# Optimization experiments

Measured on AMD Instinct MI355X. Metric: run time of the kernel, lower is better.

## Reference

```python
import jax, jax.numpy as jnp
import numpy as np

INIT_RANGE = 0.02

def setup_inputs() -> dict:
    key = jax.random.key(0)
    ks = jax.random.split(key, 5)
    B, S, D, H, Dh = 4, 2048, 768, 12, 64
    residual = jax.random.normal(ks[0], (B, S, D), dtype=jnp.float32)
    W_Q = jax.random.normal(ks[1], (H, D, Dh), dtype=jnp.float32) * INIT_RANGE
    W_K = jax.random.normal(ks[2], (H, D, Dh), dtype=jnp.float32) * INIT_RANGE
    W_V = jax.random.normal(ks[3], (H, D, Dh), dtype=jnp.float32) * INIT_RANGE
    W_O = jax.random.normal(ks[4], (H, Dh, D), dtype=jnp.float32) * INIT_RANGE
    b_Q = jnp.zeros((H, Dh), dtype=jnp.float32)
    b_K = jnp.zeros((H, Dh), dtype=jnp.float32)
    b_V = jnp.zeros((H, Dh), dtype=jnp.float32)
    b_O = jnp.zeros((D,), dtype=jnp.float32)
    return {"residual": residual, "W_Q": W_Q, "W_K": W_K, "W_V": W_V,
            "W_O": W_O, "b_Q": b_Q, "b_K": b_K, "b_V": b_V, "b_O": b_O}

def reference(residual, W_Q, W_K, W_V, W_O, b_Q, b_K, b_V, b_O):
    # residual: [b, s, d]; W_{Q,K,V}: [h, d, dh]; W_O: [h, dh, d]
    d_head = W_Q.shape[-1]
    q = jnp.einsum('bsd,hde->bshe', residual, W_Q) + b_Q  # [b, s, h, dh]
    k = jnp.einsum('bsd,hde->bshe', residual, W_K) + b_K
    v = jnp.einsum('bsd,hde->bshe', residual, W_V) + b_V
    scores = jnp.einsum('bqhe,bkhe->bhqk', q, k) / jnp.sqrt(jnp.float32(d_head))
    S = residual.shape[1]
    causal = jnp.tril(jnp.ones((S, S), dtype=bool))  # True where attending allowed
    scores = jnp.where(causal, scores, -jnp.inf)
    pattern = jax.nn.softmax(scores, axis=-1)  # [b, h, q, k]
    z = jnp.einsum('bkhe,bhqk->bqhe', v, pattern)  # [b, q, h, dh]
    attn_out = jnp.einsum('bqhe,hed->bqd', z, W_O) + b_O
    return attn_out
```

## Files before the change

kernel.cpp:

```cpp
#include <hip/hip_runtime.h>

typedef short short8 __attribute__((ext_vector_type(8)));
typedef float floatx4 __attribute__((ext_vector_type(4)));
typedef unsigned short ushort_t;


__device__ inline ushort_t f2bf(float f) {
  union { float f; unsigned u; } x; x.f = f;
  unsigned u = x.u;
  unsigned r = u + 0x7fffu + ((u >> 16) & 1u);
  return (ushort_t)(r >> 16);
}

__device__ inline unsigned cvtpk(float a, float b) {
  unsigned r;
  asm("v_cvt_pk_bf16_f32 %0, %1, %2" : "=v"(r) : "v"(a), "v"(b));
  return r;
}

__device__ inline float fexp2(float x) {
#if __has_builtin(__builtin_amdgcn_exp2f)
  return __builtin_amdgcn_exp2f(x);
#else
  return exp2f(x);
#endif
}

__device__ inline void async16(const void* g, void* l) {
  __builtin_amdgcn_global_load_lds((const __attribute__((address_space(1))) void*)g,
                                   (__attribute__((address_space(3))) void*)l,
                                   16, 0, 0);
}


__global__ __launch_bounds__(256) void conv_prep(
    const float* __restrict__ x, ushort_t* __restrict__ rx,
    const float* __restrict__ wq, const float* __restrict__ wk, const float* __restrict__ wv,
    const float* __restrict__ wo,
    const float* __restrict__ bq, const float* __restrict__ bk, const float* __restrict__ bv,
    ushort_t* __restrict__ wqkvT, ushort_t* __restrict__ woT, float* __restrict__ bqkv)
{
  __shared__ ushort_t t[64 * 72];
  const int tid = threadIdx.x;
  const int bid0 = blockIdx.x;
  if (bid0 < 6144) {
    int i = bid0 * 256 + tid;
    float4 f = ((const float4*)x)[i];
    ushort4 o;
    o.x = f2bf(f.x); o.y = f2bf(f.y); o.z = f2bf(f.z); o.w = f2bf(f.w);
    ((ushort4*)rx)[i] = o;
    return;
  }
  const int bid = bid0 - 6144;
  if (bid < 432) {
    int m = bid / 144, rem = bid % 144;
    int h = rem / 12, dt = rem % 12;
    int d0 = dt * 64;
    const float* w = (m == 0) ? wq : ((m == 1) ? wk : wv);
    const float* src = w + ((size_t)h * 768 + d0) * 64;
#pragma unroll
    for (int i = 0; i < 4; ++i) {
      int task = i * 256 + tid;
      int row = task >> 4, c4 = task & 15;
      float4 f = *(const float4*)(src + row * 64 + c4 * 4);
      ushort4 o4;
      o4.x = f2bf(f.x); o4.y = f2bf(f.y); o4.z = f2bf(f.z); o4.w = f2bf(f.w);
      *(ushort4*)&t[row * 72 + c4 * 4] = o4;
    }
    __syncthreads();
    ushort_t* dst = wqkvT + ((size_t)m * 768 + h * 64) * 768 + d0;
#pragma unroll
    for (int i = 0; i < 2; ++i) {
      int task = i * 256 + tid;
      int e = task >> 3, sc = task & 7;
      short8 d8;
#pragma unroll
      for (int j = 0; j < 8; ++j) d8[j] = (short)t[(sc * 8 + j) * 72 + e];
      *(short8*)(dst + (size_t)e * 768 + sc * 8) = d8;
    }
  } else if (bid < 576) {
    int b2 = bid - 432;
    int het = b2 / 12, dt = b2 % 12;
    int he0 = het * 64, d0 = dt * 64;
    const float* src = wo + (size_t)he0 * 768 + d0;
#pragma unroll
    for (int i = 0; i < 4; ++i) {
      int task = i * 256 + tid;
      int row = task >> 4, c4 = task & 15;
      float4 f = *(const float4*)(src + (size_t)row * 768 + c4 * 4);
      ushort4 o4;
      o4.x = f2bf(f.x); o4.y = f2bf(f.y); o4.z = f2bf(f.z); o4.w = f2bf(f.w);
      *(ushort4*)&t[row * 72 + c4 * 4] = o4;
    }
    __syncthreads();
    ushort_t* dst = woT + (size_t)d0 * 768 + he0;
#pragma unroll
    for (int i = 0; i < 2; ++i) {
      int task = i * 256 + tid;
      int dd = task >> 3, sc = task & 7;
      short8 d8;
#pragma unroll
      for (int j = 0; j < 8; ++j) d8[j] = (short)t[(sc * 8 + j) * 72 + dd];
      *(short8*)(dst + (size_t)dd * 768 + sc * 8) = d8;
    }
  } else {
    for (int idx = tid; idx < 2304; idx += 256) {
      int m = idx / 768, rem = idx - m * 768;
      const float* bp = (m == 0) ? bq : ((m == 1) ? bk : bv);
      bqkv[idx] = bp[rem];
    }
  }
}


__global__ __launch_bounds__(256) void gemm_qkv(
    const ushort_t* __restrict__ A, const ushort_t* __restrict__ Bt,
    const float* __restrict__ bias,
    ushort_t* __restrict__ q, ushort_t* __restrict__ k, ushort_t* __restrict__ vt)
{
  __shared__ ushort_t sh[17408];
  const int tid = threadIdx.x;
  const int wave = tid >> 6, lane = tid & 63;
  const int ln15 = lane & 15, quad = lane >> 4;
  const int id = blockIdx.x;
  const int xk = id & 7, j = id >> 3;
  const int bx = (xk >> 1) * 16 + (j & 15);
  const int by = (xk & 1) * 9 + (j >> 4);
  const int row0 = bx * 128, col0 = by * 128;
  const int wm = (wave >> 1) * 64, wn = (wave & 1) * 64;
  const int c0 = wave * 2;

  const ushort_t* gA0 = A + (size_t)(row0 + c0 * 16 + (lane >> 2)) * 768 + (lane & 3) * 8;
  const ushort_t* gB0 = Bt + (size_t)(col0 + c0 * 16 + (lane >> 2)) * 768 + (lane & 3) * 8;

  floatx4 acc[4][4];
#pragma unroll
  for (int mi = 0; mi < 4; ++mi)
#pragma unroll
    for (int ni = 0; ni < 4; ++ni)
      acc[mi][ni] = (floatx4){0.f, 0.f, 0.f, 0.f};

  async16(gA0, &sh[c0 * 512]);
  async16(gA0 + 16 * 768, &sh[c0 * 512 + 512]);
  async16(gB0, &sh[8192 + c0 * 512]);
  async16(gB0 + 16 * 768, &sh[8192 + c0 * 512 + 512]);
  __syncthreads();

  for (int kt = 0; kt < 24; ++kt) {
    const int buf = kt & 1;
    if (kt + 1 < 24) {
      ushort_t* dA = &sh[(buf ^ 1) * 4096];
      ushort_t* dB = &sh[8192 + (buf ^ 1) * 4096];
      async16(gA0 + (kt + 1) * 32, dA + c0 * 512);
      async16(gA0 + (kt + 1) * 32 + 16 * 768, dA + c0 * 512 + 512);
      async16(gB0 + (kt + 1) * 32, dB + c0 * 512);
      async16(gB0 + (kt + 1) * 32 + 16 * 768, dB + c0 * 512 + 512);
    }
    const ushort_t* sA = &sh[buf * 4096];
    const ushort_t* sB = &sh[8192 + buf * 4096];
    short8 af[4], bfv[4];
#pragma unroll
    for (int mi = 0; mi < 4; ++mi)
      af[mi] = *(const short8*)&sA[(wm + mi * 16 + ln15) * 32 + quad * 8];
#pragma unroll
    for (int ni = 0; ni < 4; ++ni)
      bfv[ni] = *(const short8*)&sB[(wn + ni * 16 + ln15) * 32 + quad * 8];
#pragma unroll
    for (int mi = 0; mi < 4; ++mi)
#pragma unroll
      for (int ni = 0; ni < 4; ++ni)
        acc[mi][ni] = __builtin_amdgcn_mfma_f32_16x16x32_bf16(af[mi], bfv[ni], acc[mi][ni], 0, 0, 0);
    __syncthreads();
  }

  if (col0 < 1536) {
    const float qscale = 0.125f * 1.44269504f;
#pragma unroll
    for (int mi = 0; mi < 4; ++mi) {
#pragma unroll
      for (int ni = 0; ni < 4; ++ni) {
        int gr = row0 + wm + mi * 16 + quad * 4;
        int gc = col0 + wn + ni * 16 + ln15;
        float bia = bias[gc];
        int m = gc / 768;
        int rem = gc - m * 768;
        int h = rem >> 6, e = rem & 63;
        ushort_t* dp = (m == 0) ? q : k;
#pragma unroll
        for (int r = 0; r < 4; ++r) {
          float val = acc[mi][ni][r] + bia;
          int rr = gr + r;
          int bb = rr >> 11, ss = rr & 2047;
          size_t dst = ((size_t)((bb * 12 + h) * 2048 + ss) << 6) + e;
          dp[dst] = f2bf((m == 0) ? val * qscale : val);
        }
      }
    }
  } else {
#pragma unroll
    for (int mi = 0; mi < 4; ++mi) {
#pragma unroll
      for (int ni = 0; ni < 4; ++ni) {
        int col = wn + ni * 16 + ln15;
        int rowb = wm + mi * 16 + quad * 4;
        float bia = bias[col0 + col];
        ushort4 w4;
        w4.x = f2bf(acc[mi][ni][0] + bia);
        w4.y = f2bf(acc[mi][ni][1] + bia);
        w4.z = f2bf(acc[mi][ni][2] + bia);
        w4.w = f2bf(acc[mi][ni][3] + bia);
        *(ushort4*)&sh[col * 136 + rowb] = w4;
      }
    }
    __syncthreads();
    const int relc0 = col0 - 1536;
    const int bb = row0 >> 11, s0 = row0 & 2047;
#pragma unroll
    for (int i = 0; i < 8; ++i) {
      int g = i * 256 + tid;
      int col = g >> 4, chunk = g & 15;
      short8 d = *(const short8*)&sh[col * 136 + chunk * 8];
      int hh = (relc0 + col) >> 6;
      int ee = col & 63;
      *(short8*)(vt + (((size_t)(bb * 12 + hh) * 64 + ee) << 11) + s0 + chunk * 8) = d;
    }
  }
}


__global__ __launch_bounds__(256) void gemm_out(
    const ushort_t* __restrict__ A, const ushort_t* __restrict__ Bt,
    const float* __restrict__ bias, float* __restrict__ outf)
{
  __shared__ ushort_t lA[2][64 * 32];
  __shared__ ushort_t lB[2][128 * 32];
  const int tid = threadIdx.x;
  const int wave = tid >> 6, lane = tid & 63;
  const int ln15 = lane & 15, quad = lane >> 4;
  const int id = blockIdx.x;
  const int xk = id & 7, j = id >> 3;
  const int bx = xk * 16 + (j & 15);
  const int by = j >> 4;
  const int row0 = bx * 64, col0 = by * 128;
  const int wm = (wave >> 1) * 32, wn = (wave & 1) * 64;
  const int cb = wave * 2;

  const ushort_t* gA0 = A + (size_t)(row0 + wave * 16 + (lane >> 2)) * 768 + (lane & 3) * 8;
  const ushort_t* gB0 = Bt + (size_t)(col0 + cb * 16 + (lane >> 2)) * 768 + (lane & 3) * 8;

  floatx4 acc[2][4];
#pragma unroll
  for (int mi = 0; mi < 2; ++mi)
#pragma unroll
    for (int ni = 0; ni < 4; ++ni)
      acc[mi][ni] = (floatx4){0.f, 0.f, 0.f, 0.f};

  async16(gA0, &lA[0][wave * 512]);
  async16(gB0, &lB[0][cb * 512]);
  async16(gB0 + 16 * 768, &lB[0][cb * 512 + 512]);
  __syncthreads();

  for (int kt = 0; kt < 24; ++kt) {
    const int buf = kt & 1;
    if (kt + 1 < 24) {
      async16(gA0 + (kt + 1) * 32, &lA[buf ^ 1][wave * 512]);
      async16(gB0 + (kt + 1) * 32, &lB[buf ^ 1][cb * 512]);
      async16(gB0 + (kt + 1) * 32 + 16 * 768, &lB[buf ^ 1][cb * 512 + 512]);
    }
    short8 af[2], bfv[4];
#pragma unroll
    for (int mi = 0; mi < 2; ++mi)
      af[mi] = *(const short8*)&lA[buf][(wm + mi * 16 + ln15) * 32 + quad * 8];
#pragma unroll
    for (int ni = 0; ni < 4; ++ni)
      bfv[ni] = *(const short8*)&lB[buf][(wn + ni * 16 + ln15) * 32 + quad * 8];
#pragma unroll
    for (int mi = 0; mi < 2; ++mi)
#pragma unroll
      for (int ni = 0; ni < 4; ++ni)
        acc[mi][ni] = __builtin_amdgcn_mfma_f32_16x16x32_bf16(af[mi], bfv[ni], acc[mi][ni], 0, 0, 0);
    __syncthreads();
  }

#pragma unroll
  for (int mi = 0; mi < 2; ++mi) {
#pragma unroll
    for (int ni = 0; ni < 4; ++ni) {
      int gr = row0 + wm + mi * 16 + quad * 4;
      int gc = col0 + wn + ni * 16 + ln15;
      float bia = bias[gc];
#pragma unroll
      for (int r = 0; r < 4; ++r)
        outf[(size_t)(gr + r) * 768 + gc] = acc[mi][ni][r] + bia;
    }
  }
}


__device__ inline short8 frag_ld(const ushort_t* t, int row, int ch) {
  return *(const short8*)&t[row * 64 + (((ch ^ row) & 7) * 8)];
}

__global__ __launch_bounds__(256) void attn3(
    const ushort_t* __restrict__ Q, const ushort_t* __restrict__ K,
    const ushort_t* __restrict__ VT, ushort_t* __restrict__ Z)
{
  __shared__ ushort_t lK[2][64 * 64];
  __shared__ ushort_t lV[2][64 * 64];
  const int tid = threadIdx.x;
  const int wave = tid >> 6, lane = tid & 63;
  const int ln15 = lane & 15, quad = lane >> 4;
  const int bi = blockIdx.x;
  const int bh = bi % 48;
  const int t = 15 - (bi / 48);
  const int h = bh % 12, b = bh / 12;
  const size_t base = (size_t)bh * 2048 * 64;
  const ushort_t* Qp = Q + base + (size_t)t * 128 * 64;
  const ushort_t* Kp = K + base;
  const ushort_t* Vp = VT + base;
  const int nk = 2 * t + 2;

  const int srow = tid >> 3, slch = tid & 7;
  const int sc_ = slch ^ (srow & 7);
  const int krow = (srow & 3) | ((srow & 0x0C) << 1) | ((srow & 0x10) >> 2);

#pragma unroll
  for (int i = 0; i < 4; ++i) {
    int task = i * 256 + tid;
    int row = task >> 3;
    int c = slch ^ (row & 7);
    ushort_t* qdst = (row < 64) ? &lK[1][row * 64 + slch * 8]
                                : &lV[1][(row - 64) * 64 + slch * 8];
    async16(Qp + row * 64 + c * 8, qdst);
  }
  async16(Kp + (size_t)krow * 64 + sc_ * 8, &lK[0][tid * 8]);
  async16(Kp + (size_t)(krow + 32) * 64 + sc_ * 8, &lK[0][(256 + tid) * 8]);
  async16(Vp + (size_t)srow * 2048 + sc_ * 8, &lV[0][tid * 8]);
  async16(Vp + (size_t)(srow + 32) * 2048 + sc_ * 8, &lV[0][(256 + tid) * 8]);

  const ushort_t* kPre0 = Kp + (size_t)(64 + krow) * 64 + sc_ * 8;
  const ushort_t* kPre1 = kPre0 + 32 * 64;
  const ushort_t* vPre0 = Vp + (size_t)srow * 2048 + 64 + sc_ * 8;
  const ushort_t* vPre1 = vPre0 + 32 * 2048;

  __syncthreads();
  const ushort_t* qbase = (wave < 2) ? &lK[1][0] : &lV[1][0];
  const int qrl = (wave & 1) * 32;
  short8 qf[2][2];
#pragma unroll
  for (int c = 0; c < 2; ++c) {
    qf[c][0] = frag_ld(qbase, qrl + c * 16 + ln15, quad);
    qf[c][1] = frag_ld(qbase, qrl + c * 16 + ln15, quad + 4);
  }
  __syncthreads();

  float l_i[2] = {0.f, 0.f};
  floatx4 o[2][4];
#pragma unroll
  for (int c = 0; c < 2; ++c)
#pragma unroll
    for (int et = 0; et < 4; ++et) o[c][et] = (floatx4){0.f, 0.f, 0.f, 0.f};

  const int qg0 = t * 128 + wave * 32 + ln15;

  for (int kt = 0; kt < nk; ++kt) {
    const int buf = kt & 1;
    if (kt + 1 < nk) {
      ushort_t* dK = lK[buf ^ 1];
      ushort_t* dV = lV[buf ^ 1];
      async16(kPre0, dK + tid * 8);
      async16(kPre1, dK + (256 + tid) * 8);
      async16(vPre0, dV + tid * 8);
      async16(vPre1, dV + (256 + tid) * 8);
      kPre0 += 4096; kPre1 += 4096; vPre0 += 64; vPre1 += 64;
    }

    floatx4 st[2][4];
#pragma unroll
    for (int ni = 0; ni < 4; ++ni) {
      short8 kf0 = frag_ld(lK[buf], ni * 16 + ln15, quad);
      short8 kf1 = frag_ld(lK[buf], ni * 16 + ln15, quad + 4);
#pragma unroll
      for (int c = 0; c < 2; ++c) {
        floatx4 z4 = (floatx4){0.f, 0.f, 0.f, 0.f};
        z4 = __builtin_amdgcn_mfma_f32_16x16x32_bf16(kf0, qf[c][0], z4, 0, 0, 0);
        st[c][ni] = __builtin_amdgcn_mfma_f32_16x16x32_bf16(kf1, qf[c][1], z4, 0, 0, 0);
      }
    }

    const bool masked = (kt >= 2 * t);
    short8 pf[2][2];
#pragma unroll
    for (int c = 0; c < 2; ++c) {
      const int qg = qg0 + c * 16;
      float p[16];
      float rs = 0.f;
#pragma unroll
      for (int ni = 0; ni < 4; ++ni) {
#pragma unroll
        for (int r = 0; r < 4; ++r) {
          float x = st[c][ni][r];
          if (masked) {
            int kg = kt * 64 + (ni >> 1) * 32 + quad * 8 + (ni & 1) * 4 + r;
            x = (kg <= qg) ? x : -1e30f;
          }
          p[ni * 4 + r] = fexp2(x);
        }
        rs += (p[ni * 4 + 0] + p[ni * 4 + 1]) + (p[ni * 4 + 2] + p[ni * 4 + 3]);
      }
      rs += __shfl_xor(rs, 16);
      rs += __shfl_xor(rs, 32);
      l_i[c] += rs;
      union { unsigned u[4]; short8 s8; } w0, w1;
#pragma unroll
      for (int i2 = 0; i2 < 4; ++i2) {
        w0.u[i2] = cvtpk(p[i2 * 2], p[i2 * 2 + 1]);
        w1.u[i2] = cvtpk(p[8 + i2 * 2], p[8 + i2 * 2 + 1]);
      }
      pf[c][0] = w0.s8;
      pf[c][1] = w1.s8;
    }

#pragma unroll
    for (int et = 0; et < 4; ++et) {
      short8 vf0 = frag_ld(lV[buf], et * 16 + ln15, quad);
      short8 vf1 = frag_ld(lV[buf], et * 16 + ln15, quad + 4);
#pragma unroll
      for (int c = 0; c < 2; ++c) {
        o[c][et] = __builtin_amdgcn_mfma_f32_16x16x32_bf16(vf0, pf[c][0], o[c][et], 0, 0, 0);
        o[c][et] = __builtin_amdgcn_mfma_f32_16x16x32_bf16(vf1, pf[c][1], o[c][et], 0, 0, 0);
      }
    }
    __syncthreads();
  }

#pragma unroll
  for (int c = 0; c < 2; ++c) {
    float inv = 1.f / l_i[c];
    size_t zrow = (size_t)(b * 2048 + t * 128 + wave * 32 + c * 16 + ln15);
#pragma unroll
    for (int et = 0; et < 4; ++et) {
      ushort4 w;
      w.x = f2bf(o[c][et][0] * inv);
      w.y = f2bf(o[c][et][1] * inv);
      w.z = f2bf(o[c][et][2] * inv);
      w.w = f2bf(o[c][et][3] * inv);
      *(ushort4*)&Z[zrow * 768 + h * 64 + et * 16 + quad * 4] = w;
    }
  }
}


extern "C" void kernel_launch(void* const* d_in, const int* in_sizes, int n_in,
                              void* d_out, int out_size, void* d_ws, size_t ws_size,
                              hipStream_t stream)
{
  const float* residual = (const float*)d_in[0];
  const float* W_Q = (const float*)d_in[1];
  const float* W_K = (const float*)d_in[2];
  const float* W_V = (const float*)d_in[3];
  const float* W_O = (const float*)d_in[4];
  const float* b_Q = (const float*)d_in[5];
  const float* b_K = (const float*)d_in[6];
  const float* b_V = (const float*)d_in[7];
  const float* b_O = (const float*)d_in[8];
  float* out = (float*)d_out;

  char* w = (char*)d_ws;
  ushort_t* rx    = (ushort_t*)(w + 0);
  ushort_t* wqkvT = (ushort_t*)(w + 12582912);
  ushort_t* woT   = (ushort_t*)(w + 16121856);
  float*    bqkv  = (float*)   (w + 17301504);
  ushort_t* q     = (ushort_t*)(w + 17310720);
  ushort_t* k     = (ushort_t*)(w + 29893632);
  ushort_t* vt    = (ushort_t*)(w + 55059456);
  ushort_t* z     = rx;

  conv_prep<<<6721, 256, 0, stream>>>(residual, rx, W_Q, W_K, W_V, W_O,
                                      b_Q, b_K, b_V, wqkvT, woT, bqkv);
  gemm_qkv<<<1152, 256, 0, stream>>>(rx, wqkvT, bqkv, q, k, vt);
  attn3<<<768, 256, 0, stream>>>(q, k, vt, z);
  gemm_out<<<768, 256, 0, stream>>>(z, woT, b_O, out);
}
```

Baseline: 210.0 us.

## Double GEMM K-tile to 64 and XOR-swizzle LDS layouts in projection kernels

Both the QKV and output projection GEMMs now stage 64-wide K tiles instead of 32, halving the main-loop iteration and barrier count. The shared-memory tiles use an XOR swizzle of 16-byte chunks, applied to the global load addresses and to the fragment reads, to avoid LDS bank conflicts. The V-transpose staging buffer drops its padding in favour of a swizzled layout. In exchange, LDS usage per block grows, which may reduce occupancy.

```diff
diff --git a/kernel.cpp b/kernel.cpp
--- a/kernel.cpp
+++ b/kernel.cpp
@@ -118,7 +118,7 @@
     const float* __restrict__ bias,
     ushort_t* __restrict__ q, ushort_t* __restrict__ k, ushort_t* __restrict__ vt)
 {
-  __shared__ ushort_t sh[17408];
+  __shared__ __align__(16) ushort_t sh[32768];
   const int tid = threadIdx.x;
   const int wave = tid >> 6, lane = tid & 63;
   const int ln15 = lane & 15, quad = lane >> 4;
@@ -128,10 +128,17 @@
   const int by = (xk & 1) * 9 + (j >> 4);
   const int row0 = bx * 128, col0 = by * 128;
   const int wm = (wave >> 1) * 64, wn = (wave & 1) * 64;
-  const int c0 = wave * 2;
-
-  const ushort_t* gA0 = A + (size_t)(row0 + c0 * 16 + (lane >> 2)) * 768 + (lane & 3) * 8;
-  const ushort_t* gB0 = Bt + (size_t)(col0 + c0 * 16 + (lane >> 2)) * 768 + (lane & 3) * 8;
+
+  const int sr = tid >> 3;
+  const int sc = (tid & 7) ^ (sr & 7);
+  const ushort_t* gA0 = A + (size_t)(row0 + sr) * 768 + sc * 8;
+  const ushort_t* gB0 = Bt + (size_t)(col0 + sr) * 768 + sc * 8;
+
+  const int l7 = ln15 & 7;
+  const int baA = (wm + ln15) * 64;
+  const int baB = (wn + ln15) * 64;
+  const int sl0 = (quad ^ l7) * 8;
+  const int sl1 = ((quad + 4) ^ l7) * 8;
 
   floatx4 acc[4][4];
 #pragma unroll
@@ -140,36 +147,46 @@
     for (int ni = 0; ni < 4; ++ni)
       acc[mi][ni] = (floatx4){0.f, 0.f, 0.f, 0.f};
 
-  async16(gA0, &sh[c0 * 512]);
-  async16(gA0 + 16 * 768, &sh[c0 * 512 + 512]);
-  async16(gB0, &sh[8192 + c0 * 512]);
-  async16(gB0 + 16 * 768, &sh[8192 + c0 * 512 + 512]);
+#pragma unroll
+  for (int i = 0; i < 4; ++i) {
+    async16(gA0 + i * 32 * 768, &sh[(i * 256 + tid) * 8]);
+    async16(gB0 + i * 32 * 768, &sh[16384 + (i * 256 + tid) * 8]);
+  }
   __syncthreads();
 
-  for (int kt = 0; kt < 24; ++kt) {
+  for (int kt = 0; kt < 12; ++kt) {
     const int buf = kt & 1;
-    if (kt + 1 < 24) {
-      ushort_t* dA = &sh[(buf ^ 1) * 4096];
-      ushort_t* dB = &sh[8192 + (buf ^ 1) * 4096];
-      async16(gA0 + (kt + 1) * 32, dA + c0 * 512);
-      async16(gA0 + (kt + 1) * 32 + 16 * 768, dA + c0 * 512 + 512);
-      async16(gB0 + (kt + 1) * 32, dB + c0 * 512);
-      async16(gB0 + (kt + 1) * 32 + 16 * 768, dB + c0 * 512 + 512);
-    }
-    const ushort_t* sA = &sh[buf * 4096];
-    const ushort_t* sB = &sh[8192 + buf * 4096];
-    short8 af[4], bfv[4];
+    if (kt + 1 < 12) {
+      ushort_t* dA = &sh[(buf ^ 1) * 8192];
+      ushort_t* dB = &sh[16384 + (buf ^ 1) * 8192];
+      const ushort_t* ga = gA0 + (kt + 1) * 64;
+      const ushort_t* gb = gB0 + (kt + 1) * 64;
+#pragma unroll
+      for (int i = 0; i < 4; ++i) {
+        async16(ga + i * 32 * 768, dA + (i * 256 + tid) * 8);
+        async16(gb + i * 32 * 768, dB + (i * 256 + tid) * 8);
+      }
+    }
+    const ushort_t* sA = &sh[buf * 8192];
+    const ushort_t* sB = &sh[16384 + buf * 8192];
+    short8 af[4][2], bfv[4][2];
+#pragma unroll
+    for (int mi = 0; mi < 4; ++mi) {
+      af[mi][0] = *(const short8*)&sA[baA + mi * 1024 + sl0];
+      af[mi][1] = *(const short8*)&sA[baA + mi * 1024 + sl1];
+    }
+#pragma unroll
+    for (int ni = 0; ni < 4; ++ni) {
+      bfv[ni][0] = *(const short8*)&sB[baB + ni * 1024 + sl0];
+      bfv[ni][1] = *(const short8*)&sB[baB + ni * 1024 + sl1];
+    }
 #pragma unroll
     for (int mi = 0; mi < 4; ++mi)
-      af[mi] = *(const short8*)&sA[(wm + mi * 16 + ln15) * 32 + quad * 8];
-#pragma unroll
-    for (int ni = 0; ni < 4; ++ni)
-      bfv[ni] = *(const short8*)&sB[(wn + ni * 16 + ln15) * 32 + quad * 8];
-#pragma unroll
-    for (int mi = 0; mi < 4; ++mi)
-#pragma unroll
-      for (int ni = 0; ni < 4; ++ni)
-        acc[mi][ni] = __builtin_amdgcn_mfma_f32_16x16x32_bf16(af[mi], bfv[ni], acc[mi][ni], 0, 0, 0);
+#pragma unroll
+      for (int ni = 0; ni < 4; ++ni) {
+        acc[mi][ni] = __builtin_amdgcn_mfma_f32_16x16x32_bf16(af[mi][0], bfv[ni][0], acc[mi][ni], 0, 0, 0);
+        acc[mi][ni] = __builtin_amdgcn_mfma_f32_16x16x32_bf16(af[mi][1], bfv[ni][1], acc[mi][ni], 0, 0, 0);
+      }
     __syncthreads();
   }
 
@@ -203,13 +220,15 @@
       for (int ni = 0; ni < 4; ++ni) {
         int col = wn + ni * 16 + ln15;
         int rowb = wm + mi * 16 + quad * 4;
+        int rowc = rowb >> 2;
+        int msw = (col & 7) << 2;
         float bia = bias[col0 + col];
         ushort4 w4;
         w4.x = f2bf(acc[mi][ni][0] + bia);
         w4.y = f2bf(acc[mi][ni][1] + bia);
         w4.z = f2bf(acc[mi][ni][2] + bia);
         w4.w = f2bf(acc[mi][ni][3] + bia);
-        *(ushort4*)&sh[col * 136 + rowb] = w4;
+        *(ushort4*)&sh[col * 128 + ((rowc ^ msw) << 2)] = w4;
       }
     }
     __syncthreads();
@@ -219,7 +238,8 @@
     for (int i = 0; i < 8; ++i) {
       int g = i * 256 + tid;
       int col = g >> 4, chunk = g & 15;
-      short8 d = *(const short8*)&sh[col * 136 + chunk * 8];
+      int msw = (col & 7) << 2;
+      short8 d = *(const short8*)&sh[col * 128 + (((chunk * 2) ^ msw) << 2)];
       int hh = (relc0 + col) >> 6;
       int ee = col & 63;
       *(short8*)(vt + (((size_t)(bb * 12 + hh) * 64 + ee) << 11) + s0 + chunk * 8) = d;
@@ -232,8 +252,7 @@
     const ushort_t* __restrict__ A, const ushort_t* __restrict__ Bt,
     const float* __restrict__ bias, float* __restrict__ outf)
 {
-  __shared__ ushort_t lA[2][64 * 32];
-  __shared__ ushort_t lB[2][128 * 32];
+  __shared__ __align__(16) ushort_t sh[24576];
   const int tid = threadIdx.x;
   const int wave = tid >> 6, lane = tid & 63;
   const int ln15 = lane & 15, quad = lane >> 4;
@@ -243,10 +262,17 @@
   const int by = j >> 4;
   const int row0 = bx * 64, col0 = by * 128;
   const int wm = (wave >> 1) * 32, wn = (wave & 1) * 64;
-  const int cb = wave * 2;
-
-  const ushort_t* gA0 = A + (size_t)(row0 + wave * 16 + (lane >> 2)) * 768 + (lane & 3) * 8;
-  const ushort_t* gB0 = Bt + (size_t)(col0 + cb * 16 + (lane >> 2)) * 768 + (lane & 3) * 8;
+
+  const int sr = tid >> 3;
+  const int sc = (tid & 7) ^ (sr & 7);
+  const ushort_t* gA0 = A + (size_t)(row0 + sr) * 768 + sc * 8;
+  const ushort_t* gB0 = Bt + (size_t)(col0 + sr) * 768 + sc * 8;
+
+  const int l7 = ln15 & 7;
+  const int baA = (wm + ln15) * 64;
+  const int baB = (wn + ln15) * 64;
+  const int sl0 = (quad ^ l7) * 8;
+  const int sl1 = ((quad + 4) ^ l7) * 8;
 
   floatx4 acc[2][4];
 #pragma unroll
@@ -255,30 +281,48 @@
     for (int ni = 0; ni < 4; ++ni)
       acc[mi][ni] = (floatx4){0.f, 0.f, 0.f, 0.f};
 
-  async16(gA0, &lA[0][wave * 512]);
-  async16(gB0, &lB[0][cb * 512]);
-  async16(gB0 + 16 * 768, &lB[0][cb * 512 + 512]);
+#pragma unroll
+  for (int i = 0; i < 2; ++i)
+    async16(gA0 + i * 32 * 768, &sh[(i * 256 + tid) * 8]);
+#pragma unroll
+  for (int i = 0; i < 4; ++i)
+    async16(gB0 + i * 32 * 768, &sh[8192 + (i * 256 + tid) * 8]);
   __syncthreads();
 
-  for (int kt = 0; kt < 24; ++kt) {
+  for (int kt = 0; kt < 12; ++kt) {
     const int buf = kt & 1;
-    if (kt + 1 < 24) {
-      async16(gA0 + (kt + 1) * 32, &lA[buf ^ 1][wave * 512]);
-      async16(gB0 + (kt + 1) * 32, &lB[buf ^ 1][cb * 512]);
-      async16(gB0 + (kt + 1) * 32 + 16 * 768, &lB[buf ^ 1][cb * 512 + 512]);
-    }
-    short8 af[2], bfv[4];
+    if (kt + 1 < 12) {
+      ushort_t* dA = &sh[(buf ^ 1) * 4096];
+      ushort_t* dB = &sh[8192 + (buf ^ 1) * 8192];
+      const ushort_t* ga = gA0 + (kt + 1) * 64;
+      const ushort_t* gb = gB0 + (kt + 1) * 64;
+#pragma unroll
+      for (int i = 0; i < 2; ++i)
+        async16(ga + i * 32 * 768, dA + (i * 256 + tid) * 8);
+#pragma unroll
+      for (int i = 0; i < 4; ++i)
+        async16(gb + i * 32 * 768, dB + (i * 256 + tid) * 8);
+    }
+    const ushort_t* sA = &sh[buf * 4096];
+    const ushort_t* sB = &sh[8192 + buf * 8192];
+    short8 af[2][2], bfv[4][2];
+#pragma unroll
+    for (int mi = 0; mi < 2; ++mi) {
+      af[mi][0] = *(const short8*)&sA[baA + mi * 1024 + sl0];
+      af[mi][1] = *(const short8*)&sA[baA + mi * 1024 + sl1];
+    }
+#pragma unroll
+    for (int ni = 0; ni < 4; ++ni) {
+      bfv[ni][0] = *(const short8*)&sB[baB + ni * 1024 + sl0];
+      bfv[ni][1] = *(const short8*)&sB[baB + ni * 1024 + sl1];
+    }
 #pragma unroll
     for (int mi = 0; mi < 2; ++mi)
-      af[mi] = *(const short8*)&lA[buf][(wm + mi * 16 + ln15) * 32 + quad * 8];
-#pragma unroll
-    for (int ni = 0; ni < 4; ++ni)
-      bfv[ni] = *(const short8*)&lB[buf][(wn + ni * 16 + ln15) * 32 + quad * 8];
-#pragma unroll
-    for (int mi = 0; mi < 2; ++mi)
-#pragma unroll
-      for (int ni = 0; ni < 4; ++ni)
-        acc[mi][ni] = __builtin_amdgcn_mfma_f32_16x16x32_bf16(af[mi], bfv[ni], acc[mi][ni], 0, 0, 0);
+#pragma unroll
+      for (int ni = 0; ni < 4; ++ni) {
+        acc[mi][ni] = __builtin_amdgcn_mfma_f32_16x16x32_bf16(af[mi][0], bfv[ni][0], acc[mi][ni], 0, 0, 0);
+        acc[mi][ni] = __builtin_amdgcn_mfma_f32_16x16x32_bf16(af[mi][1], bfv[ni][1], acc[mi][ni], 0, 0, 0);
+      }
     __syncthreads();
   }
 
```

New measurement: 192.3 us. 1.09x faster.
